# Optimization experiments

Hardware: AMD Instinct MI355X
Metric: run time of the kernel (lower is better)

Reference implementation:

```python
import jax, jax.numpy as jnp
import numpy as np

H = 128          # hidden_dim
E = 1048576      # num edges
N = 262144       # num nodes
T = 4096         # num targets / subgraphs
NET = 8          # num_edge_types
SCALAR_DIM = 32  # max(H // 4, 8)
SHORT = 1.0      # short_time_scale
LONG = 24.0      # long_time_scale


def _ln(x):
    # F.layer_norm without affine params, eps=1e-5, biased variance
    m = jnp.mean(x, axis=-1, keepdims=True)
    v = jnp.var(x, axis=-1, keepdims=True)
    return (x - m) / jnp.sqrt(v + 1e-5)


def _seg_wmean(vals, gid, w, num_groups):
    # masked/weighted segment mean: mask is folded into w (zeros drop rows)
    num = jax.ops.segment_sum(vals * w[:, None], gid, num_segments=num_groups)
    den = jax.ops.segment_sum(w, gid, num_segments=num_groups)
    return num / jnp.maximum(den, 1e-6)[:, None]


def setup_inputs():
    key = jax.random.key(0)
    ks = jax.random.split(key, 14)
    node_repr = jax.random.normal(ks[0], (N, H), jnp.float32)
    edge_repr = jax.random.normal(ks[1], (E, H), jnp.float32)
    edge_src = jax.random.randint(ks[2], (E,), 0, N)
    edge_subgraph_id = jax.random.randint(ks[3], (E,), 0, T)
    node_subgraph_id = jax.random.randint(ks[4], (N,), 0, T)
    node_hop_depth = jax.random.randint(ks[5], (N,), 1, 4)
    rel_ids = jax.random.randint(ks[6], (E,), 0, 2 * NET)
    edge_relative_time = jax.random.uniform(ks[7], (E,), jnp.float32) * 48.0
    target_local_idx = jnp.arange(T, dtype=jnp.int32)
    base_dst = jax.random.randint(ks[8], (E,), 0, N)
    hit = jax.random.uniform(ks[9], (E,)) < 0.25
    edge_dst = jnp.where(hit, target_local_idx[edge_subgraph_id], base_dst)
    # scalar_proj: Linear(8, 32); fuse: Linear(8*H+32, 2*H) -> GELU -> Linear(2*H, H)
    W1 = jax.random.normal(ks[10], (8, SCALAR_DIM), jnp.float32) / np.sqrt(8.0)
    b1 = jnp.zeros((SCALAR_DIM,), jnp.float32)
    W2 = jax.random.normal(ks[11], (8 * H + SCALAR_DIM, 2 * H), jnp.float32) / np.sqrt(8.0 * H + SCALAR_DIM)
    b2 = jnp.zeros((2 * H,), jnp.float32)
    W3 = jax.random.normal(ks[12], (2 * H, H), jnp.float32) / np.sqrt(2.0 * H)
    b3 = jnp.zeros((H,), jnp.float32)
    return dict(node_repr=node_repr, edge_repr=edge_repr, edge_src=edge_src,
                edge_dst=edge_dst, rel_ids=rel_ids, edge_relative_time=edge_relative_time,
                target_local_idx=target_local_idx, node_subgraph_id=node_subgraph_id,
                edge_subgraph_id=edge_subgraph_id, node_hop_depth=node_hop_depth,
                W1=W1, b1=b1, W2=W2, b2=b2, W3=W3, b3=b3)


def reference(node_repr, edge_repr, edge_src, edge_dst, rel_ids, edge_relative_time,
              target_local_idx, node_subgraph_id, edge_subgraph_id, node_hop_depth,
              W1, b1, W2, b2, W3, b3):
    dtype = node_repr.dtype
    t = edge_relative_time.astype(dtype)
    short_w = jnp.exp(-t / SHORT)
    long_w = jnp.exp(-t / LONG)

    tmask = (edge_dst == target_local_idx[edge_subgraph_id]).astype(dtype)   # target edges
    in_m = tmask * (rel_ids < NET).astype(dtype)                             # inbound
    out_m = tmask * (rel_ids >= NET).astype(dtype)                           # outbound

    esg = edge_subgraph_id
    in_short = _seg_wmean(edge_repr, esg, in_m * short_w, T)
    out_short = _seg_wmean(edge_repr, esg, out_m * short_w, T)
    in_long = _seg_wmean(edge_repr, esg, in_m * long_w, T)
    out_long = _seg_wmean(edge_repr, esg, out_m * long_w, T)

    hop1_m = (node_hop_depth == 1).astype(dtype)
    hop2_m = (node_hop_depth >= 2).astype(dtype)
    hop1_mean_raw = _seg_wmean(node_repr, node_subgraph_id, hop1_m, T)
    hop2_mean_raw = _seg_wmean(node_repr, node_subgraph_id, hop2_m, T)

    src_repr = node_repr[edge_src]  # [E, H] gather
    hop1_edges_short = _seg_wmean(src_repr, esg, tmask * short_w, T)
    hop1_edges_long = _seg_wmean(src_repr, esg, tmask * long_w, T)

    burst_delta = _ln(in_short + out_short - (in_long + out_long))
    direction_gap = _ln(out_long - in_long)
    hop_gap = _ln(hop1_mean_raw - hop2_mean_raw)
    short_long_gap = _ln(hop1_edges_short - hop1_edges_long)
    asymmetry = _ln(jnp.abs(direction_gap))
    hop1_mean = _ln(hop1_mean_raw)
    hop2_mean = _ln(hop2_mean_raw)
    risk_base = _ln(in_long + out_long)

    seg1 = lambda w, g: jax.ops.segment_sum(w, g, num_segments=T)
    target_edge_count = seg1(tmask, esg)
    edge_time_mean = seg1(t * tmask, esg) / jnp.maximum(target_edge_count, 1e-6)
    inbound_count = seg1(in_m, esg)
    outbound_count = seg1(out_m, esg)
    hop1_count = seg1(hop1_m, node_subgraph_id)
    hop2_count = seg1(hop2_m, node_subgraph_id)
    short_mass = seg1(tmask * short_w, esg)
    long_mass = seg1(tmask * long_w, esg)

    scalar_features = jnp.stack([
        jnp.log1p(inbound_count), jnp.log1p(outbound_count),
        jnp.log1p(hop1_count), jnp.log1p(hop2_count),
        edge_time_mean, short_mass, long_mass, short_mass - long_mass], axis=-1)  # [T, 8]

    scalar_embedding = jax.nn.gelu(scalar_features @ W1 + b1, approximate=False)
    fused_input = jnp.concatenate([burst_delta, direction_gap, hop_gap, short_long_gap,
                                   asymmetry, hop1_mean, hop2_mean, risk_base,
                                   scalar_embedding], axis=-1)  # [T, 8*H + 32]
    hidden = jax.nn.gelu(fused_input @ W2 + b2, approximate=False)
    risk_embedding = 0.25 * jnp.tanh(hidden @ W3 + b3)  # [T, H]

    hop_gap_norm = jnp.mean(jnp.linalg.norm(hop_gap, axis=-1))
    sl_gap_norm = jnp.mean(jnp.linalg.norm(short_long_gap, axis=-1))
    dir_gap_norm = jnp.mean(jnp.linalg.norm(direction_gap, axis=-1))
    return risk_embedding, hop_gap_norm, sl_gap_norm, dir_gap_norm
```

## Files before the change

kernel.cpp:

```cpp
#include <hip/hip_runtime.h>
#include <math.h>

#define HDIM 128
#define TDIM 4096
#define NET_T 8

__device__ __forceinline__ float wave_sum64(float v) {
#pragma unroll
  for (int d = 32; d > 0; d >>= 1) v += __shfl_xor(v, d, 64);
  return v;
}

__device__ __forceinline__ float gelu_exact(float x) {
  return 0.5f * x * (1.0f + erff(x * 0.70710678118654752440f));
}

struct LN2 { float zx, zy, norm; };

__device__ __forceinline__ LN2 ln128(float x0, float x1) {
  float s = wave_sum64(x0 + x1);
  float mean = s * (1.0f / 128.0f);
  float d0 = x0 - mean, d1 = x1 - mean;
  float sq = wave_sum64(d0 * d0 + d1 * d1);
  float var = sq * (1.0f / 128.0f);
  float rstd = rsqrtf(var + 1e-5f);
  LN2 r;
  r.zx = d0 * rstd;
  r.zy = d1 * rstd;
  r.norm = sqrtf(sq) * rstd;
  return r;
}

__global__ void count_kernel(const int* __restrict__ edge_dst,
                             const int* __restrict__ esg,
                             const int* __restrict__ tli,
                             const int* __restrict__ nsg,
                             int* __restrict__ ecnt, int* __restrict__ ncnt,
                             int E_, int N_) {
  int gid = blockIdx.x * blockDim.x + threadIdx.x;
  if (gid < E_) {
    int s = esg[gid];
    if (edge_dst[gid] == tli[s]) atomicAdd(&ecnt[s], 1);
  }
  if (gid < N_) {
    atomicAdd(&ncnt[nsg[gid]], 1);
  }
}

__global__ __launch_bounds__(64) void scan_kernel(
    const int* __restrict__ ecnt, int* __restrict__ eoff, int* __restrict__ ecur,
    const int* __restrict__ ncnt, int* __restrict__ noff, int* __restrict__ ncur) {
  const int* cnt;
  int *off, *cur;
  if (blockIdx.x == 0) { cnt = ecnt; off = eoff; cur = ecur; }
  else                 { cnt = ncnt; off = noff; cur = ncur; }
  int lane = threadIdx.x;
  int base = lane * 64;
  int s = 0;
  for (int i = 0; i < 64; i++) s += cnt[base + i];
  int incl = s;
#pragma unroll
  for (int d = 1; d < 64; d <<= 1) {
    int v = __shfl_up(incl, d, 64);
    if (lane >= d) incl += v;
  }
  int run = incl - s;
  for (int i = 0; i < 64; i++) {
    off[base + i] = run;
    cur[base + i] = run;
    run += cnt[base + i];
  }
}

__global__ void scatter_kernel(const int* __restrict__ edge_dst,
                               const int* __restrict__ esg,
                               const int* __restrict__ tli,
                               const int* __restrict__ edge_src,
                               const int* __restrict__ rel_ids,
                               const float* __restrict__ etime,
                               const int* __restrict__ nsg,
                               const int* __restrict__ depth,
                               int* __restrict__ ecur, int* __restrict__ ncur,
                               int* __restrict__ s_eid, int* __restrict__ s_srcpk,
                               float* __restrict__ s_t, int* __restrict__ s_npk,
                               int E_, int N_) {
  int gid = blockIdx.x * blockDim.x + threadIdx.x;
  if (gid < E_) {
    int sg = esg[gid];
    if (edge_dst[gid] == tli[sg]) {
      int pos = atomicAdd(&ecur[sg], 1);
      s_eid[pos] = gid;
      s_srcpk[pos] = (edge_src[gid] << 1) | (rel_ids[gid] < NET_T ? 1 : 0);
      s_t[pos] = etime[gid];
    }
  }
  if (gid < N_) {
    int sg = nsg[gid];
    int pos = atomicAdd(&ncur[sg], 1);
    s_npk[pos] = (gid << 1) | (depth[gid] == 1 ? 1 : 0);
  }
}

__global__ __launch_bounds__(256) void target_kernel(
    const float* __restrict__ node_repr, const float* __restrict__ edge_repr,
    const int* __restrict__ eoff, const int* __restrict__ ecnt,
    const int* __restrict__ noff, const int* __restrict__ ncnt,
    const int* __restrict__ s_eid, const int* __restrict__ s_srcpk,
    const float* __restrict__ s_t, const int* __restrict__ s_npk,
    const float* __restrict__ W1, const float* __restrict__ b1,
    float* __restrict__ fused, float* __restrict__ norm_acc) {
  const int t = blockIdx.x;
  const int tid = threadIdx.x;
  const int w = tid >> 6;
  const int lane = tid & 63;
  const int e0 = eoff[t], ec = ecnt[t];
  const int n0 = noff[t], nc = ncnt[t];

  __shared__ float lse[2][6][128];
  __shared__ float lss[2][6];
  __shared__ float lsn[2][2][128];
  __shared__ float lnc[2];

  const int co = 2 * lane;

  if (w < 2) {
    float ais0 = 0, ais1 = 0, aos0 = 0, aos1 = 0;
    float ail0 = 0, ail1 = 0, aol0 = 0, aol1 = 0;
    float hs0 = 0, hs1 = 0, hl0 = 0, hl1 = 0;
    float d_is = 0, d_os = 0, d_il = 0, d_ol = 0, tsum = 0, cin = 0;

#define EDGE_BODY(ii)                                                          \
    {                                                                          \
      int eid = s_eid[ii];                                                     \
      int pk = s_srcpk[ii];                                                    \
      float tt = s_t[ii];                                                      \
      int src = pk >> 1;                                                       \
      const float2 er = *(const float2*)(edge_repr + (size_t)eid * HDIM + co);\
      const float2 nr = *(const float2*)(node_repr + (size_t)src * HDIM + co);\
      float sw = expf(-tt);                                                    \
      float lw = expf(-tt * (1.0f / 24.0f));                                   \
      float fin = (float)(pk & 1);                                             \
      float wis = fin * sw, wos = sw - wis;                                    \
      float wil = fin * lw, wol = lw - wil;                                    \
      ais0 += er.x * wis; ais1 += er.y * wis;                                  \
      aos0 += er.x * wos; aos1 += er.y * wos;                                  \
      ail0 += er.x * wil; ail1 += er.y * wil;                                  \
      aol0 += er.x * wol; aol1 += er.y * wol;                                  \
      hs0 += nr.x * sw; hs1 += nr.y * sw;                                      \
      hl0 += nr.x * lw; hl1 += nr.y * lw;                                      \
      d_is += wis; d_os += wos; d_il += wil; d_ol += wol;                      \
      tsum += tt; cin += fin;                                                  \
    }

    int i = e0 + w;
    const int end = e0 + ec;
    for (; i + 2 < end; i += 4) { EDGE_BODY(i); EDGE_BODY(i + 2); }
    if (i < end) EDGE_BODY(i);
#undef EDGE_BODY

    lse[w][0][co] = ais0; lse[w][0][co + 1] = ais1;
    lse[w][1][co] = aos0; lse[w][1][co + 1] = aos1;
    lse[w][2][co] = ail0; lse[w][2][co + 1] = ail1;
    lse[w][3][co] = aol0; lse[w][3][co + 1] = aol1;
    lse[w][4][co] = hs0;  lse[w][4][co + 1] = hs1;
    lse[w][5][co] = hl0;  lse[w][5][co + 1] = hl1;
    if (lane == 0) {
      lss[w][0] = d_is; lss[w][1] = d_os; lss[w][2] = d_il;
      lss[w][3] = d_ol; lss[w][4] = tsum; lss[w][5] = cin;
    }
  } else {
    const int w2 = w - 2;
    float h10 = 0, h11 = 0, h20 = 0, h21 = 0, c1 = 0;

#define NODE_BODY(ii)                                                          \
    {                                                                          \
      int pk = s_npk[ii];                                                      \
      int idx = pk >> 1;                                                       \
      const float2 nr = *(const float2*)(node_repr + (size_t)idx * HDIM + co);\
      float f1 = (float)(pk & 1);                                              \
      h10 += nr.x * f1;          h11 += nr.y * f1;                             \
      h20 += nr.x * (1.0f - f1); h21 += nr.y * (1.0f - f1);                    \
      c1 += f1;                                                                \
    }

    int i = n0 + w2;
    const int end = n0 + nc;
    for (; i + 2 < end; i += 4) { NODE_BODY(i); NODE_BODY(i + 2); }
    if (i < end) NODE_BODY(i);
#undef NODE_BODY

    lsn[w2][0][co] = h10; lsn[w2][0][co + 1] = h11;
    lsn[w2][1][co] = h20; lsn[w2][1][co + 1] = h21;
    if (lane == 0) lnc[w2] = c1;
  }

  __syncthreads();
  if (w != 0) return;

  float ais0 = lse[0][0][co] + lse[1][0][co], ais1 = lse[0][0][co + 1] + lse[1][0][co + 1];
  float aos0 = lse[0][1][co] + lse[1][1][co], aos1 = lse[0][1][co + 1] + lse[1][1][co + 1];
  float ail0 = lse[0][2][co] + lse[1][2][co], ail1 = lse[0][2][co + 1] + lse[1][2][co + 1];
  float aol0 = lse[0][3][co] + lse[1][3][co], aol1 = lse[0][3][co + 1] + lse[1][3][co + 1];
  float hs0  = lse[0][4][co] + lse[1][4][co], hs1  = lse[0][4][co + 1] + lse[1][4][co + 1];
  float hl0  = lse[0][5][co] + lse[1][5][co], hl1  = lse[0][5][co + 1] + lse[1][5][co + 1];
  float h10  = lsn[0][0][co] + lsn[1][0][co], h11  = lsn[0][0][co + 1] + lsn[1][0][co + 1];
  float h20  = lsn[0][1][co] + lsn[1][1][co], h21  = lsn[0][1][co + 1] + lsn[1][1][co + 1];
  float d_is = lss[0][0] + lss[1][0];
  float d_os = lss[0][1] + lss[1][1];
  float d_il = lss[0][2] + lss[1][2];
  float d_ol = lss[0][3] + lss[1][3];
  float tsum = lss[0][4] + lss[1][4];
  float cin  = lss[0][5] + lss[1][5];
  float c1   = lnc[0] + lnc[1];
  float c2 = (float)nc - c1;

  float r_is = 1.0f / fmaxf(d_is, 1e-6f);
  float r_os = 1.0f / fmaxf(d_os, 1e-6f);
  float r_il = 1.0f / fmaxf(d_il, 1e-6f);
  float r_ol = 1.0f / fmaxf(d_ol, 1e-6f);
  float sm = d_is + d_os;
  float lm = d_il + d_ol;
  float r_sm = 1.0f / fmaxf(sm, 1e-6f);
  float r_lm = 1.0f / fmaxf(lm, 1e-6f);
  float r_c1 = 1.0f / fmaxf(c1, 1e-6f);
  float r_c2 = 1.0f / fmaxf(c2, 1e-6f);

  float mis0 = ais0 * r_is, mis1 = ais1 * r_is;
  float mos0 = aos0 * r_os, mos1 = aos1 * r_os;
  float mil0 = ail0 * r_il, mil1 = ail1 * r_il;
  float mol0 = aol0 * r_ol, mol1 = aol1 * r_ol;
  float mhs0 = hs0 * r_sm, mhs1 = hs1 * r_sm;
  float mhl0 = hl0 * r_lm, mhl1 = hl1 * r_lm;
  float mh10 = h10 * r_c1, mh11 = h11 * r_c1;
  float mh20 = h20 * r_c2, mh21 = h21 * r_c2;

  LN2 z_burst = ln128(mis0 + mos0 - mil0 - mol0, mis1 + mos1 - mil1 - mol1);
  LN2 z_dgap  = ln128(mol0 - mil0, mol1 - mil1);
  LN2 z_hgap  = ln128(mh10 - mh20, mh11 - mh21);
  LN2 z_sl    = ln128(mhs0 - mhl0, mhs1 - mhl1);
  LN2 z_asym  = ln128(fabsf(z_dgap.zx), fabsf(z_dgap.zy));
  LN2 z_h1    = ln128(mh10, mh11);
  LN2 z_h2    = ln128(mh20, mh21);
  LN2 z_rb    = ln128(mil0 + mol0, mil1 + mol1);

  if (lane == 0) {
    atomicAdd(&norm_acc[0], z_hgap.norm);
    atomicAdd(&norm_acc[1], z_sl.norm);
    atomicAdd(&norm_acc[2], z_dgap.norm);
  }

  float* frow = fused + (size_t)t * 1056;
  *(float2*)(frow + 0 * HDIM + co) = make_float2(z_burst.zx, z_burst.zy);
  *(float2*)(frow + 1 * HDIM + co) = make_float2(z_dgap.zx, z_dgap.zy);
  *(float2*)(frow + 2 * HDIM + co) = make_float2(z_hgap.zx, z_hgap.zy);
  *(float2*)(frow + 3 * HDIM + co) = make_float2(z_sl.zx, z_sl.zy);
  *(float2*)(frow + 4 * HDIM + co) = make_float2(z_asym.zx, z_asym.zy);
  *(float2*)(frow + 5 * HDIM + co) = make_float2(z_h1.zx, z_h1.zy);
  *(float2*)(frow + 6 * HDIM + co) = make_float2(z_h2.zx, z_h2.zy);
  *(float2*)(frow + 7 * HDIM + co) = make_float2(z_rb.zx, z_rb.zy);

  float ecf = (float)ec;
  float sf[8];
  sf[0] = log1pf(cin);
  sf[1] = log1pf(ecf - cin);
  sf[2] = log1pf(c1);
  sf[3] = log1pf(c2);
  sf[4] = tsum / fmaxf(ecf, 1e-6f);
  sf[5] = sm;
  sf[6] = lm;
  sf[7] = sm - lm;
  if (lane < 32) {
    float acc = b1[lane];
#pragma unroll
    for (int i = 0; i < 8; i++) acc += sf[i] * W1[i * 32 + lane];
    frow[1024 + lane] = gelu_exact(acc);
  }
}

template <int MODE>
__global__ __launch_bounds__(256) void gemm_kernel(
    const float* __restrict__ A, const float* __restrict__ B,
    const float* __restrict__ bias, float* __restrict__ C,
    int M, int N, int K) {
  __shared__ __align__(16) float As[32][34];
  __shared__ __align__(16) float Bs[32][68];
  const int tid = threadIdx.x;
  const int tx = tid & 15, ty = tid >> 4;
  const int m0 = blockIdx.y * 32, n0 = blockIdx.x * 64;
  float acc[2][4] = {};

  const int am = tid >> 3;
  const int ak = (tid & 7) * 4;
  const int bk = tid >> 3;
  const int bn = (tid & 7) * 8;

  for (int kt = 0; kt < K; kt += 32) {
    float4 av = *(const float4*)&A[(size_t)(m0 + am) * K + kt + ak];
    const float* bp = &B[(size_t)(kt + bk) * N + n0 + bn];
    float4 bv0 = *(const float4*)bp;
    float4 bv1 = *(const float4*)(bp + 4);
    As[ak + 0][am] = av.x;
    As[ak + 1][am] = av.y;
    As[ak + 2][am] = av.z;
    As[ak + 3][am] = av.w;
    *(float4*)&Bs[bk][bn] = bv0;
    *(float4*)&Bs[bk][bn + 4] = bv1;
    __syncthreads();
#pragma unroll
    for (int kk = 0; kk < 32; kk++) {
      float2 a2 = *(const float2*)&As[kk][ty * 2];
      float4 b4 = *(const float4*)&Bs[kk][tx * 4];
      float a[2] = {a2.x, a2.y};
      float b[4] = {b4.x, b4.y, b4.z, b4.w};
#pragma unroll
      for (int i2 = 0; i2 < 2; i2++)
#pragma unroll
        for (int j2 = 0; j2 < 4; j2++)
          acc[i2][j2] = fmaf(a[i2], b[j2], acc[i2][j2]);
    }
    __syncthreads();
  }

#pragma unroll
  for (int i2 = 0; i2 < 2; i2++) {
    int m = m0 + ty * 2 + i2;
    int n = n0 + tx * 4;
    float4 bb = *(const float4*)&bias[n];
    float4 v;
    v.x = acc[i2][0] + bb.x;
    v.y = acc[i2][1] + bb.y;
    v.z = acc[i2][2] + bb.z;
    v.w = acc[i2][3] + bb.w;
    if (MODE == 0) {
      v.x = gelu_exact(v.x); v.y = gelu_exact(v.y);
      v.z = gelu_exact(v.z); v.w = gelu_exact(v.w);
    } else {
      v.x = 0.25f * tanhf(v.x); v.y = 0.25f * tanhf(v.y);
      v.z = 0.25f * tanhf(v.z); v.w = 0.25f * tanhf(v.w);
    }
    *(float4*)&C[(size_t)m * N + n] = v;
  }
}

__global__ void finalize_kernel(const float* __restrict__ norm_acc,
                                float* __restrict__ out) {
  int i = threadIdx.x;
  if (i < 3) out[(size_t)TDIM * HDIM + i] = norm_acc[i] * (1.0f / (float)TDIM);
}

extern "C" void kernel_launch(void* const* d_in, const int* in_sizes, int n_in,
                              void* d_out, int out_size, void* d_ws, size_t ws_size,
                              hipStream_t stream) {
  const float* node_repr = (const float*)d_in[0];
  const float* edge_repr = (const float*)d_in[1];
  const int* edge_src = (const int*)d_in[2];
  const int* edge_dst = (const int*)d_in[3];
  const int* rel_ids = (const int*)d_in[4];
  const float* etime = (const float*)d_in[5];
  const int* tli = (const int*)d_in[6];
  const int* nsg = (const int*)d_in[7];
  const int* esg = (const int*)d_in[8];
  const int* depth = (const int*)d_in[9];
  const float* W1 = (const float*)d_in[10];
  const float* b1 = (const float*)d_in[11];
  const float* W2 = (const float*)d_in[12];
  const float* b2 = (const float*)d_in[13];
  const float* W3 = (const float*)d_in[14];
  const float* b3 = (const float*)d_in[15];
  float* out = (float*)d_out;

  const int E_ = in_sizes[2];
  const int N_ = in_sizes[7];

  char* ws = (char*)d_ws;
  size_t off = 0;
  auto alloc = [&](size_t bytes) -> void* {
    off = (off + 255) & ~(size_t)255;
    void* p = ws + off;
    off += bytes;
    return p;
  };
  int* ecnt = (int*)alloc((size_t)TDIM * 4);
  int* eoff = (int*)alloc((size_t)TDIM * 4);
  int* ecur = (int*)alloc((size_t)TDIM * 4);
  int* ncnt = (int*)alloc((size_t)TDIM * 4);
  int* noff = (int*)alloc((size_t)TDIM * 4);
  int* ncur = (int*)alloc((size_t)TDIM * 4);
  int* s_eid = (int*)alloc((size_t)E_ * 4);
  int* s_srcpk = (int*)alloc((size_t)E_ * 4);
  float* s_t = (float*)alloc((size_t)E_ * 4);
  int* s_npk = (int*)alloc((size_t)N_ * 4);
  float* fused = (float*)alloc((size_t)TDIM * 1056 * 4);
  float* hidden = (float*)alloc((size_t)TDIM * 256 * 4);
  float* norm_acc = (float*)alloc(4 * 4);

  hipMemsetAsync(ecnt, 0, (size_t)TDIM * 4, stream);
  hipMemsetAsync(ncnt, 0, (size_t)TDIM * 4, stream);
  hipMemsetAsync(norm_acc, 0, 16, stream);

  int gmax = (E_ > N_ ? E_ : N_);
  int g1 = (gmax + 255) / 256;

  count_kernel<<<g1, 256, 0, stream>>>(edge_dst, esg, tli, nsg, ecnt, ncnt, E_, N_);
  scan_kernel<<<2, 64, 0, stream>>>(ecnt, eoff, ecur, ncnt, noff, ncur);
  scatter_kernel<<<g1, 256, 0, stream>>>(edge_dst, esg, tli, edge_src, rel_ids,
                                         etime, nsg, depth, ecur, ncur,
                                         s_eid, s_srcpk, s_t, s_npk, E_, N_);
  target_kernel<<<TDIM, 256, 0, stream>>>(node_repr, edge_repr, eoff, ecnt, noff,
                                          ncnt, s_eid, s_srcpk, s_t, s_npk,
                                          W1, b1, fused, norm_acc);
  gemm_kernel<0><<<dim3(256 / 64, TDIM / 32), 256, 0, stream>>>(
      fused, W2, b2, hidden, TDIM, 256, 8 * HDIM + 32);
  gemm_kernel<1><<<dim3(HDIM / 64, TDIM / 32), 256, 0, stream>>>(
      hidden, W3, b3, out, TDIM, HDIM, 256);
  finalize_kernel<<<1, 64, 0, stream>>>(norm_acc, out);
}
```

Baseline: 988.7 us.

## Split edge and node gathers across all four waves with shuffle-broadcast indices

Each of the four waves in the per-target block now processes a contiguous quarter of both the edge list and the node list, instead of two waves doing edges and two doing nodes. Per-edge index, time and weight loads plus the exp calls are done once per lane for a 64-entry chunk and broadcast with shuffles, so redundant scalar loads and exps are removed from the inner loop. The three norm atomics are replaced by a per-target buffer reduced deterministically in a wider finalize kernel. This balances load between edge and node work, at the cost of more shared memory and shuffle traffic.

New measurement: 899.5 us. 9.0% less time.

```diff
diff --git a/kernel.cpp b/kernel.cpp
--- a/kernel.cpp
+++ b/kernel.cpp
@@ -108,111 +108,133 @@
     const int* __restrict__ s_eid, const int* __restrict__ s_srcpk,
     const float* __restrict__ s_t, const int* __restrict__ s_npk,
     const float* __restrict__ W1, const float* __restrict__ b1,
-    float* __restrict__ fused, float* __restrict__ norm_acc) {
+    float* __restrict__ fused, float* __restrict__ normbuf) {
   const int t = blockIdx.x;
   const int tid = threadIdx.x;
   const int w = tid >> 6;
   const int lane = tid & 63;
   const int e0 = eoff[t], ec = ecnt[t];
   const int n0 = noff[t], nc = ncnt[t];
-
-  __shared__ float lse[2][6][128];
-  __shared__ float lss[2][6];
-  __shared__ float lsn[2][2][128];
-  __shared__ float lnc[2];
-
   const int co = 2 * lane;
 
-  if (w < 2) {
+  __shared__ float lse[4][6][128];
+  __shared__ float lss[4][6];
+  __shared__ float lsn[4][2][128];
+  __shared__ float lnc[4];
+
+  {
+    const int cbeg = e0 + ((ec * w) >> 2);
+    const int cend = e0 + ((ec * (w + 1)) >> 2);
     float ais0 = 0, ais1 = 0, aos0 = 0, aos1 = 0;
     float ail0 = 0, ail1 = 0, aol0 = 0, aol1 = 0;
     float hs0 = 0, hs1 = 0, hl0 = 0, hl1 = 0;
     float d_is = 0, d_os = 0, d_il = 0, d_ol = 0, tsum = 0, cin = 0;
 
-#define EDGE_BODY(ii)                                                          \
-    {                                                                          \
-      int eid = s_eid[ii];                                                     \
-      int pk = s_srcpk[ii];                                                    \
-      float tt = s_t[ii];                                                      \
-      int src = pk >> 1;                                                       \
-      const float2 er = *(const float2*)(edge_repr + (size_t)eid * HDIM + co);\
-      const float2 nr = *(const float2*)(node_repr + (size_t)src * HDIM + co);\
-      float sw = expf(-tt);                                                    \
-      float lw = expf(-tt * (1.0f / 24.0f));                                   \
-      float fin = (float)(pk & 1);                                             \
-      float wis = fin * sw, wos = sw - wis;                                    \
-      float wil = fin * lw, wol = lw - wil;                                    \
-      ais0 += er.x * wis; ais1 += er.y * wis;                                  \
-      aos0 += er.x * wos; aos1 += er.y * wos;                                  \
-      ail0 += er.x * wil; ail1 += er.y * wil;                                  \
-      aol0 += er.x * wol; aol1 += er.y * wol;                                  \
-      hs0 += nr.x * sw; hs1 += nr.y * sw;                                      \
-      hl0 += nr.x * lw; hl1 += nr.y * lw;                                      \
-      d_is += wis; d_os += wos; d_il += wil; d_ol += wol;                      \
-      tsum += tt; cin += fin;                                                  \
-    }
-
-    int i = e0 + w;
-    const int end = e0 + ec;
-    for (; i + 2 < end; i += 4) { EDGE_BODY(i); EDGE_BODY(i + 2); }
-    if (i < end) EDGE_BODY(i);
-#undef EDGE_BODY
-
+    for (int base = cbeg; base < cend; base += 64) {
+      int n = cend - base;
+      if (n > 64) n = 64;
+      int p_eid = 0, p_pk = 0;
+      float p_sw = 0.0f, p_lw = 0.0f;
+      if (lane < n) {
+        int idx = base + lane;
+        p_eid = s_eid[idx];
+        p_pk = s_srcpk[idx];
+        float tt = s_t[idx];
+        p_sw = expf(-tt);
+        p_lw = expf(-tt * (1.0f / 24.0f));
+        float fin = (float)(p_pk & 1);
+        float wis = fin * p_sw, wil = fin * p_lw;
+        d_is += wis; d_os += p_sw - wis;
+        d_il += wil; d_ol += p_lw - wil;
+        tsum += tt; cin += fin;
+      }
+#pragma unroll 2
+      for (int j = 0; j < n; ++j) {
+        int eid = __shfl(p_eid, j, 64);
+        int pk = __shfl(p_pk, j, 64);
+        float sw = __shfl(p_sw, j, 64);
+        float lw = __shfl(p_lw, j, 64);
+        int src = pk >> 1;
+        float fin = (float)(pk & 1);
+        const float2 er = *(const float2*)(edge_repr + (size_t)eid * HDIM + co);
+        const float2 nr = *(const float2*)(node_repr + (size_t)src * HDIM + co);
+        float wis = fin * sw, wos = sw - wis;
+        float wil = fin * lw, wol = lw - wil;
+        ais0 = fmaf(er.x, wis, ais0); ais1 = fmaf(er.y, wis, ais1);
+        aos0 = fmaf(er.x, wos, aos0); aos1 = fmaf(er.y, wos, aos1);
+        ail0 = fmaf(er.x, wil, ail0); ail1 = fmaf(er.y, wil, ail1);
+        aol0 = fmaf(er.x, wol, aol0); aol1 = fmaf(er.y, wol, aol1);
+        hs0 = fmaf(nr.x, sw, hs0); hs1 = fmaf(nr.y, sw, hs1);
+        hl0 = fmaf(nr.x, lw, hl0); hl1 = fmaf(nr.y, lw, hl1);
+      }
+    }
     lse[w][0][co] = ais0; lse[w][0][co + 1] = ais1;
     lse[w][1][co] = aos0; lse[w][1][co + 1] = aos1;
     lse[w][2][co] = ail0; lse[w][2][co + 1] = ail1;
     lse[w][3][co] = aol0; lse[w][3][co + 1] = aol1;
     lse[w][4][co] = hs0;  lse[w][4][co + 1] = hs1;
     lse[w][5][co] = hl0;  lse[w][5][co + 1] = hl1;
+    d_is = wave_sum64(d_is); d_os = wave_sum64(d_os);
+    d_il = wave_sum64(d_il); d_ol = wave_sum64(d_ol);
+    tsum = wave_sum64(tsum); cin = wave_sum64(cin);
     if (lane == 0) {
       lss[w][0] = d_is; lss[w][1] = d_os; lss[w][2] = d_il;
       lss[w][3] = d_ol; lss[w][4] = tsum; lss[w][5] = cin;
     }
-  } else {
-    const int w2 = w - 2;
+  }
+
+  {
+    const int cbeg = n0 + ((nc * w) >> 2);
+    const int cend = n0 + ((nc * (w + 1)) >> 2);
     float h10 = 0, h11 = 0, h20 = 0, h21 = 0, c1 = 0;
 
-#define NODE_BODY(ii)                                                          \
-    {                                                                          \
-      int pk = s_npk[ii];                                                      \
-      int idx = pk >> 1;                                                       \
-      const float2 nr = *(const float2*)(node_repr + (size_t)idx * HDIM + co);\
-      float f1 = (float)(pk & 1);                                              \
-      h10 += nr.x * f1;          h11 += nr.y * f1;                             \
-      h20 += nr.x * (1.0f - f1); h21 += nr.y * (1.0f - f1);                    \
-      c1 += f1;                                                                \
-    }
-
-    int i = n0 + w2;
-    const int end = n0 + nc;
-    for (; i + 2 < end; i += 4) { NODE_BODY(i); NODE_BODY(i + 2); }
-    if (i < end) NODE_BODY(i);
-#undef NODE_BODY
-
-    lsn[w2][0][co] = h10; lsn[w2][0][co + 1] = h11;
-    lsn[w2][1][co] = h20; lsn[w2][1][co + 1] = h21;
-    if (lane == 0) lnc[w2] = c1;
+    for (int base = cbeg; base < cend; base += 64) {
+      int n = cend - base;
+      if (n > 64) n = 64;
+      int p_pk = 0;
+      if (lane < n) {
+        p_pk = s_npk[base + lane];
+        c1 += (float)(p_pk & 1);
+      }
+#pragma unroll 2
+      for (int j = 0; j < n; ++j) {
+        int pk = __shfl(p_pk, j, 64);
+        int idx = pk >> 1;
+        float f1 = (float)(pk & 1);
+        float f2 = 1.0f - f1;
+        const float2 nr = *(const float2*)(node_repr + (size_t)idx * HDIM + co);
+        h10 = fmaf(nr.x, f1, h10); h11 = fmaf(nr.y, f1, h11);
+        h20 = fmaf(nr.x, f2, h20); h21 = fmaf(nr.y, f2, h21);
+      }
+    }
+    lsn[w][0][co] = h10; lsn[w][0][co + 1] = h11;
+    lsn[w][1][co] = h20; lsn[w][1][co + 1] = h21;
+    c1 = wave_sum64(c1);
+    if (lane == 0) lnc[w] = c1;
   }
 
   __syncthreads();
   if (w != 0) return;
 
-  float ais0 = lse[0][0][co] + lse[1][0][co], ais1 = lse[0][0][co + 1] + lse[1][0][co + 1];
-  float aos0 = lse[0][1][co] + lse[1][1][co], aos1 = lse[0][1][co + 1] + lse[1][1][co + 1];
-  float ail0 = lse[0][2][co] + lse[1][2][co], ail1 = lse[0][2][co + 1] + lse[1][2][co + 1];
-  float aol0 = lse[0][3][co] + lse[1][3][co], aol1 = lse[0][3][co + 1] + lse[1][3][co + 1];
-  float hs0  = lse[0][4][co] + lse[1][4][co], hs1  = lse[0][4][co + 1] + lse[1][4][co + 1];
-  float hl0  = lse[0][5][co] + lse[1][5][co], hl1  = lse[0][5][co + 1] + lse[1][5][co + 1];
-  float h10  = lsn[0][0][co] + lsn[1][0][co], h11  = lsn[0][0][co + 1] + lsn[1][0][co + 1];
-  float h20  = lsn[0][1][co] + lsn[1][1][co], h21  = lsn[0][1][co + 1] + lsn[1][1][co + 1];
-  float d_is = lss[0][0] + lss[1][0];
-  float d_os = lss[0][1] + lss[1][1];
-  float d_il = lss[0][2] + lss[1][2];
-  float d_ol = lss[0][3] + lss[1][3];
-  float tsum = lss[0][4] + lss[1][4];
-  float cin  = lss[0][5] + lss[1][5];
-  float c1   = lnc[0] + lnc[1];
+  float v0[6], v1[6];
+#pragma unroll
+  for (int k = 0; k < 6; ++k) {
+    v0[k] = lse[0][k][co] + lse[1][k][co] + lse[2][k][co] + lse[3][k][co];
+    v1[k] = lse[0][k][co + 1] + lse[1][k][co + 1] + lse[2][k][co + 1] + lse[3][k][co + 1];
+  }
+  float dsc[6];
+#pragma unroll
+  for (int k = 0; k < 6; ++k)
+    dsc[k] = lss[0][k] + lss[1][k] + lss[2][k] + lss[3][k];
+  float h10 = lsn[0][0][co] + lsn[1][0][co] + lsn[2][0][co] + lsn[3][0][co];
+  float h11 = lsn[0][0][co + 1] + lsn[1][0][co + 1] + lsn[2][0][co + 1] + lsn[3][0][co + 1];
+  float h20 = lsn[0][1][co] + lsn[1][1][co] + lsn[2][1][co] + lsn[3][1][co];
+  float h21 = lsn[0][1][co + 1] + lsn[1][1][co + 1] + lsn[2][1][co + 1] + lsn[3][1][co + 1];
+  float c1 = lnc[0] + lnc[1] + lnc[2] + lnc[3];
   float c2 = (float)nc - c1;
+
+  float d_is = dsc[0], d_os = dsc[1], d_il = dsc[2], d_ol = dsc[3];
+  float tsum = dsc[4], cin = dsc[5];
 
   float r_is = 1.0f / fmaxf(d_is, 1e-6f);
   float r_os = 1.0f / fmaxf(d_os, 1e-6f);
@@ -225,12 +247,12 @@
   float r_c1 = 1.0f / fmaxf(c1, 1e-6f);
   float r_c2 = 1.0f / fmaxf(c2, 1e-6f);
 
-  float mis0 = ais0 * r_is, mis1 = ais1 * r_is;
-  float mos0 = aos0 * r_os, mos1 = aos1 * r_os;
-  float mil0 = ail0 * r_il, mil1 = ail1 * r_il;
-  float mol0 = aol0 * r_ol, mol1 = aol1 * r_ol;
-  float mhs0 = hs0 * r_sm, mhs1 = hs1 * r_sm;
-  float mhl0 = hl0 * r_lm, mhl1 = hl1 * r_lm;
+  float mis0 = v0[0] * r_is, mis1 = v1[0] * r_is;
+  float mos0 = v0[1] * r_os, mos1 = v1[1] * r_os;
+  float mil0 = v0[2] * r_il, mil1 = v1[2] * r_il;
+  float mol0 = v0[3] * r_ol, mol1 = v1[3] * r_ol;
+  float mhs0 = v0[4] * r_sm, mhs1 = v1[4] * r_sm;
+  float mhl0 = v0[5] * r_lm, mhl1 = v1[5] * r_lm;
   float mh10 = h10 * r_c1, mh11 = h11 * r_c1;
   float mh20 = h20 * r_c2, mh21 = h21 * r_c2;
 
@@ -244,9 +266,9 @@
   LN2 z_rb    = ln128(mil0 + mol0, mil1 + mol1);
 
   if (lane == 0) {
-    atomicAdd(&norm_acc[0], z_hgap.norm);
-    atomicAdd(&norm_acc[1], z_sl.norm);
-    atomicAdd(&norm_acc[2], z_dgap.norm);
+    normbuf[t] = z_hgap.norm;
+    normbuf[TDIM + t] = z_sl.norm;
+    normbuf[2 * TDIM + t] = z_dgap.norm;
   }
 
   float* frow = fused + (size_t)t * 1056;
@@ -342,10 +364,26 @@
   }
 }
 
-__global__ void finalize_kernel(const float* __restrict__ norm_acc,
-                                float* __restrict__ out) {
-  int i = threadIdx.x;
-  if (i < 3) out[(size_t)TDIM * HDIM + i] = norm_acc[i] * (1.0f / (float)TDIM);
+__global__ __launch_bounds__(256) void finalize_kernel(
+    const float* __restrict__ normbuf, float* __restrict__ out) {
+  const int tid = threadIdx.x;
+  const int w = tid >> 6, lane = tid & 63;
+  float s0 = 0, s1 = 0, s2 = 0;
+  for (int t = tid; t < TDIM; t += 256) {
+    s0 += normbuf[t];
+    s1 += normbuf[TDIM + t];
+    s2 += normbuf[2 * TDIM + t];
+  }
+  s0 = wave_sum64(s0);
+  s1 = wave_sum64(s1);
+  s2 = wave_sum64(s2);
+  __shared__ float red[3][4];
+  if (lane == 0) { red[0][w] = s0; red[1][w] = s1; red[2][w] = s2; }
+  __syncthreads();
+  if (tid < 3) {
+    float v = red[tid][0] + red[tid][1] + red[tid][2] + red[tid][3];
+    out[(size_t)TDIM * HDIM + tid] = v * (1.0f / (float)TDIM);
+  }
 }
 
 extern "C" void kernel_launch(void* const* d_in, const int* in_sizes, int n_in,
@@ -392,11 +430,10 @@
   int* s_npk = (int*)alloc((size_t)N_ * 4);
   float* fused = (float*)alloc((size_t)TDIM * 1056 * 4);
   float* hidden = (float*)alloc((size_t)TDIM * 256 * 4);
-  float* norm_acc = (float*)alloc(4 * 4);
+  float* normbuf = (float*)alloc((size_t)3 * TDIM * 4);
 
   hipMemsetAsync(ecnt, 0, (size_t)TDIM * 4, stream);
   hipMemsetAsync(ncnt, 0, (size_t)TDIM * 4, stream);
-  hipMemsetAsync(norm_acc, 0, 16, stream);
 
   int gmax = (E_ > N_ ? E_ : N_);
   int g1 = (gmax + 255) / 256;
@@ -408,10 +445,10 @@
                                          s_eid, s_srcpk, s_t, s_npk, E_, N_);
   target_kernel<<<TDIM, 256, 0, stream>>>(node_repr, edge_repr, eoff, ecnt, noff,
                                           ncnt, s_eid, s_srcpk, s_t, s_npk,
-                                          W1, b1, fused, norm_acc);
+                                          W1, b1, fused, normbuf);
   gemm_kernel<0><<<dim3(256 / 64, TDIM / 32), 256, 0, stream>>>(
       fused, W2, b2, hidden, TDIM, 256, 8 * HDIM + 32);
   gemm_kernel<1><<<dim3(HDIM / 64, TDIM / 32), 256, 0, stream>>>(
       hidden, W3, b3, out, TDIM, HDIM, 256);
-  finalize_kernel<<<1, 64, 0, stream>>>(norm_acc, out);
-}
+  finalize_kernel<<<1, 256, 0, stream>>>(normbuf, out);
+}
```
